# Performance work log

Hardware: AMD Instinct MI355X
Metric: run time of the kernel (lower is better)

The kernel has to match this reference:

```python
import jax, jax.numpy as jnp
import numpy as np

NJ, NS = 30000, 12000            # num job / skill nodes
E_JS, E_SJ, E_SS = 300000, 300000, 150000
SBERT, HID, OUT = 384, 128, 128
H = 2                             # GAT heads (concat=True)
NEG_SLOPE = 0.2


def setup_inputs() -> dict:
    key = jax.random.key(0)
    ks = iter(jax.random.split(key, 64))
    nrm = lambda shape, s=1.0: jax.random.normal(next(ks), shape, jnp.float32) * s
    ridx = lambda n, hi: jax.random.randint(next(ks), (n,), 0, hi, jnp.int32)
    W = 0.05  # weight scale to keep activations sane across layers
    return dict(
        x_job=nrm((NJ, SBERT)), x_skill=nrm((NS, SBERT)),
        ei_js_src=ridx(E_JS, NJ), ei_js_dst=ridx(E_JS, NS),
        ei_sj_src=ridx(E_SJ, NS), ei_sj_dst=ridx(E_SJ, NJ),
        ei_ss_src=ridx(E_SS, NS), ei_ss_dst=ridx(E_SS, NS),
        query=nrm((SBERT,)),
        W0_job=nrm((SBERT, HID), W), b0_job=jnp.zeros((HID,), jnp.float32),
        g0_job=jnp.ones((HID,), jnp.float32), be0_job=jnp.zeros((HID,), jnp.float32),
        W0_skill=nrm((SBERT, HID), W), b0_skill=jnp.zeros((HID,), jnp.float32),
        g0_skill=jnp.ones((HID,), jnp.float32), be0_skill=jnp.zeros((HID,), jnp.float32),
        gat_Ws=nrm((2, 3, HID, H * HID), W), gat_Wd=nrm((2, 3, HID, H * HID), W),
        gat_as=nrm((2, 3, H, HID), W), gat_ad=nrm((2, 3, H, HID), W),
        gat_b=jnp.zeros((2, 3, H * HID), jnp.float32),
        inter_W=nrm((2, 2, H * HID, HID), W), inter_b=jnp.zeros((2, 2, HID), jnp.float32),
        Wjf=nrm((HID, OUT), W), bjf=jnp.zeros((OUT,), jnp.float32),
        Wq=nrm((SBERT, OUT), W), bq=jnp.zeros((OUT,), jnp.float32),
    )


def _layer_norm(x, g, b):
    mu = x.mean(-1, keepdims=True)
    var = ((x - mu) ** 2).mean(-1, keepdims=True)
    return (x - mu) * jax.lax.rsqrt(var + 1e-5) * g + b


def _gat(x_src, x_dst, src, dst, Ws, Wd, a_s, a_d, bias, num_dst):
    # PyG GATConv: lin_src/lin_dst (no bias), additive attention, scatter-softmax over dst.
    hs = (x_src @ Ws).reshape(-1, H, HID)            # [Ns,H,C]
    hd = (x_dst @ Wd).reshape(-1, H, HID)            # [Nd,H,C]
    e = jax.nn.leaky_relu((hs * a_s).sum(-1)[src] + (hd * a_d).sum(-1)[dst], NEG_SLOPE)  # [E,H]
    m = jax.ops.segment_max(e, dst, num_segments=num_dst)
    p = jnp.exp(e - m[dst])
    den = jax.ops.segment_sum(p, dst, num_segments=num_dst)
    w = p / (den[dst] + 1e-16)                       # [E,H]
    out = jax.ops.segment_sum(hs[src] * w[:, :, None], dst, num_segments=num_dst)
    return out.reshape(num_dst, H * HID) + bias


def _forward(x_job, x_skill, query,
             W0_job, b0_job, g0_job, be0_job, W0_skill, b0_skill, g0_skill, be0_skill,
             gat_Ws, gat_Wd, gat_as, gat_ad, gat_b, inter_W, inter_b, Wjf, bjf, Wq, bq,
             ei_js_src, ei_js_dst, ei_sj_src, ei_sj_dst, ei_ss_src, ei_ss_dst):
    # initial per-type lin + LN + relu (dropout = identity in eval)
    xj = jax.nn.relu(_layer_norm(x_job @ W0_job + b0_job, g0_job, be0_job))
    xs = jax.nn.relu(_layer_norm(x_skill @ W0_skill + b0_skill, g0_skill, be0_skill))
    # skill->skill relation adds self loops (src == dst node type)
    loops = jnp.arange(NS, dtype=jnp.int32)
    ss_src = jnp.concatenate([ei_ss_src, loops])
    ss_dst = jnp.concatenate([ei_ss_dst, loops])
    for i in range(2):  # num_layers
        o_s = (_gat(xj, xs, ei_js_src, ei_js_dst, gat_Ws[i, 0], gat_Wd[i, 0],
                    gat_as[i, 0], gat_ad[i, 0], gat_b[i, 0], NS)
               + _gat(xs, xs, ss_src, ss_dst, gat_Ws[i, 2], gat_Wd[i, 2],
                      gat_as[i, 2], gat_ad[i, 2], gat_b[i, 2], NS))  # HeteroConv aggr='sum'
        o_j = _gat(xs, xj, ei_sj_src, ei_sj_dst, gat_Ws[i, 1], gat_Wd[i, 1],
                   gat_as[i, 1], gat_ad[i, 1], gat_b[i, 1], NJ)
        xj = jax.nn.relu(o_j @ inter_W[i, 0] + inter_b[i, 0])
        xs = jax.nn.relu(o_s @ inter_W[i, 1] + inter_b[i, 1])
    job_emb = xj @ Wjf + bjf                          # [NJ,OUT]
    q = query @ Wq + bq                               # [OUT]
    scores = job_emb @ q                              # [NJ]
    return scores, job_emb, q


def reference(x_job, x_skill, ei_js_src, ei_js_dst, ei_sj_src, ei_sj_dst,
              ei_ss_src, ei_ss_dst, query,
              W0_job, b0_job, g0_job, be0_job, W0_skill, b0_skill, g0_skill, be0_skill,
              gat_Ws, gat_Wd, gat_as, gat_ad, gat_b, inter_W, inter_b,
              Wjf, bjf, Wq, bq):
    return _forward(x_job, x_skill, query,
                    W0_job, b0_job, g0_job, be0_job, W0_skill, b0_skill, g0_skill, be0_skill,
                    gat_Ws, gat_Wd, gat_as, gat_ad, gat_b, inter_W, inter_b, Wjf, bjf, Wq, bq,
                    ei_js_src, ei_js_dst, ei_sj_src, ei_sj_dst, ei_ss_src, ei_ss_dst)
```

## Files before the change

kernel.cpp:

```cpp
#include <hip/hip_runtime.h>
#include <hip/hip_bf16.h>
#include <math.h>

#define NJ 30000
#define NS 12000
#define E_JS 300000
#define E_SJ 300000
#define E_SS 150000
#define ETOT (E_JS + E_SJ + E_SS + NS)
#define NBINS (NS + NJ + NS)
#define NBUK ((NBINS + 63) / 64)
#define SBERT 384
#define HIST_NB 512
#define SCAT_NB 120
#define CAST_MATS 10
#define CAST_BPM 48

static inline int cdiv(int a, int b) { return (a + b - 1) / b; }

typedef __attribute__((ext_vector_type(8))) short bf8_t;
typedef __attribute__((ext_vector_type(4))) float f4_t;
typedef unsigned short u16;

__device__ inline float bf2f(unsigned short u) {
    union { unsigned int i; float f; } z; z.i = ((unsigned int)u) << 16; return z.f;
}
__device__ inline unsigned short f2bf(float f) {
    unsigned int x = __float_as_uint(f);
    unsigned int r = (x + 0x7fffu + ((x >> 16) & 1u)) >> 16;
    return (unsigned short)r;
}

__device__ inline void edge_decode(int e, const int* js_src, const int* js_dst,
                                   const int* sj_src, const int* sj_dst,
                                   const int* ss_src, const int* ss_dst,
                                   int& src, int& bin) {
    if (e < E_JS) { src = js_src[e]; bin = js_dst[e]; }
    else if (e < E_JS + E_SJ) { int i = e - E_JS; src = sj_src[i]; bin = NS + sj_dst[i]; }
    else if (e < E_JS + E_SJ + E_SS) { int i = e - E_JS - E_SJ; src = ss_src[i]; bin = NS + NJ + ss_dst[i]; }
    else { int i = e - E_JS - E_SJ - E_SS; src = i; bin = NS + NJ + i; }
}

struct CastT { const float* src; unsigned short* dst; int K; int N; };
struct PrepArgs {
    CastT m[CAST_MATS];
    const float* Ws; const float* as_; const float* Wd; const float* ad_;
    float* wsa; float* wda; int* bcnt;
    const float* query; const float* Wq; const float* bq; float* qv;
};

__global__ __launch_bounds__(256) void k_prep(PrepArgs A) {
    __shared__ float ldt[32][33];
    int b = blockIdx.x;
    if (b < CAST_MATS * CAST_BPM) {
        int mi = b / CAST_BPM, bx = b % CAST_BPM;
        CastT cm = A.m[mi];
        int tilesN = cm.N >> 5;
        int total = (cm.K >> 5) * tilesN;
        if (bx >= total) return;
        int tk = bx / tilesN, tn = bx % tilesN;
        int k0 = tk * 32, n0 = tn * 32;
        int col = threadIdx.x & 31;
        int row0 = threadIdx.x >> 5;
#pragma unroll
        for (int r = 0; r < 4; ++r) {
            int kk = row0 + r * 8;
            ldt[kk][col] = cm.src[(size_t)(k0 + kk) * cm.N + n0 + col];
        }
        __syncthreads();
#pragma unroll
        for (int r = 0; r < 4; ++r) {
            int nn = row0 + r * 8;
            cm.dst[(size_t)(n0 + nn) * cm.K + k0 + col] = f2bf(ldt[col][nn]);
        }
    } else if (b < CAST_MATS * CAST_BPM + 12) {
        int id = (b - CAST_MATS * CAST_BPM) * 256 + threadIdx.x;
        if (id < NBUK) A.bcnt[id] = 0;
        if (id >= 2 * 1536) return;
        int which = id / 1536;
        int r = id % 1536;
        int lr = r / 256;
        int kh = r % 256;
        int k = kh / 2, h = kh % 2;
        const float* W = which ? A.Wd : A.Ws;
        const float* a = which ? A.ad_ : A.as_;
        const float* wrow = W + ((size_t)(lr * 128 + k)) * 256 + h * 128;
        const float* arow = a + (size_t)(lr * 2 + h) * 128;
        float acc = 0.f;
        for (int c2 = 0; c2 < 128; ++c2) acc += wrow[c2] * arow[c2];
        (which ? A.wda : A.wsa)[lr * 256 + k * 2 + h] = acc;
    } else {
        int c = threadIdx.x;
        if (c < 128) {
            float acc = A.bq[c];
            for (int k = 0; k < SBERT; ++k) acc += A.query[k] * A.Wq[(size_t)k * 128 + c];
            A.qv[c] = acc;
        }
    }
}

struct GJob {
    const void* X; const unsigned short* Wt;
    const float* bias; const float* gamma; const float* beta;
    void* Y; int M; int K; int N; int ldY; int srcf32;
    const float* qv; float* sc;
};
struct GPair { GJob a; GJob b; int blocksA; };

template <int EPI>
__device__ void mgemm_body(const GPair& P, int bx, int by) {
    int mb = bx;
    GJob g = (mb < P.blocksA) ? P.a : P.b;
    if (mb >= P.blocksA) mb -= P.blocksA;
    const int n0 = by * 128;
    if (n0 >= g.N) return;
    const int row0 = mb * 64;

    __shared__ __align__(16) unsigned short Al[64][40];
    __shared__ __align__(16) unsigned short Bl[128][40];
    const int t = threadIdx.x;
    const int wave = t >> 6, lane = t & 63;
    const int q = lane >> 4, c = lane & 15;
    const int K = g.K;

    f4_t acc[8];
#pragma unroll
    for (int nt = 0; nt < 8; ++nt) acc[nt] = (f4_t){0.f, 0.f, 0.f, 0.f};

    for (int k0 = 0; k0 < K; k0 += 32) {
#pragma unroll
        for (int it = 0; it < 3; ++it) {
            int idx = t + it * 256;
            int r = idx >> 2, cc = (idx & 3) * 8;
            if (r < 64) {
                int gr = row0 + r;
                if (g.srcf32) {
                    ushort4 lo = make_ushort4(0, 0, 0, 0), hi = lo;
                    if (gr < g.M) {
                        const float* Xf = (const float*)g.X;
                        const float* p = &Xf[(size_t)gr * K + k0 + cc];
                        float4 f0 = *(const float4*)p;
                        float4 f1 = *(const float4*)(p + 4);
                        lo = make_ushort4(f2bf(f0.x), f2bf(f0.y), f2bf(f0.z), f2bf(f0.w));
                        hi = make_ushort4(f2bf(f1.x), f2bf(f1.y), f2bf(f1.z), f2bf(f1.w));
                    }
                    *(ushort4*)&Al[r][cc] = lo;
                    *(ushort4*)&Al[r][cc + 4] = hi;
                } else {
                    const unsigned short* Xb = (const unsigned short*)g.X;
                    uint4 va = (gr < g.M) ? *(const uint4*)&Xb[(size_t)gr * K + k0 + cc]
                                          : make_uint4(0u, 0u, 0u, 0u);
                    *(uint4*)&Al[r][cc] = va;
                }
            } else {
                int br = r - 64;
                *(uint4*)&Bl[br][cc] = *(const uint4*)&g.Wt[(size_t)(n0 + br) * K + k0 + cc];
            }
        }
        __syncthreads();
        bf8_t af = *(const bf8_t*)&Al[wave * 16 + c][q * 8];
#pragma unroll
        for (int nt = 0; nt < 8; ++nt) {
            bf8_t bfr = *(const bf8_t*)&Bl[nt * 16 + c][q * 8];
            acc[nt] = __builtin_amdgcn_mfma_f32_16x16x32_bf16(af, bfr, acc[nt], 0, 0, 0);
        }
        __syncthreads();
    }

    float bcol[8], gcol[8], becol[8], qcol[8];
#pragma unroll
    for (int nt = 0; nt < 8; ++nt) {
        bcol[nt] = (EPI >= 1) ? g.bias[n0 + nt * 16 + c] : 0.f;
        if constexpr (EPI == 3) {
            gcol[nt] = g.gamma[nt * 16 + c];
            becol[nt] = g.beta[nt * 16 + c];
        }
        if constexpr (EPI == 1) qcol[nt] = g.qv[n0 + nt * 16 + c];
    }

#pragma unroll
    for (int r = 0; r < 4; ++r) {
        int grow = row0 + wave * 16 + q * 4 + r;
        float v[8];
#pragma unroll
        for (int nt = 0; nt < 8; ++nt) v[nt] = acc[nt][r] + bcol[nt];
        if constexpr (EPI == 3) {
            float s = 0.f, ss = 0.f;
#pragma unroll
            for (int nt = 0; nt < 8; ++nt) { s += v[nt]; ss += v[nt] * v[nt]; }
#pragma unroll
            for (int m = 8; m >= 1; m >>= 1) {
                s += __shfl_xor(s, m, 64);
                ss += __shfl_xor(ss, m, 64);
            }
            float mu = s * (1.f / 128.f);
            float var = ss * (1.f / 128.f) - mu * mu;
            float rs = rsqrtf(var + 1e-5f);
#pragma unroll
            for (int nt = 0; nt < 8; ++nt)
                v[nt] = fmaxf((v[nt] - mu) * rs * gcol[nt] + becol[nt], 0.f);
        } else if constexpr (EPI == 2) {
#pragma unroll
            for (int nt = 0; nt < 8; ++nt) v[nt] = fmaxf(v[nt], 0.f);
        }
        if constexpr (EPI == 1) {
            float part = 0.f;
#pragma unroll
            for (int nt = 0; nt < 8; ++nt) part += v[nt] * qcol[nt];
#pragma unroll
            for (int m = 8; m >= 1; m >>= 1) part += __shfl_xor(part, m, 64);
            if (c == 0 && grow < g.M) g.sc[grow] = part;
        }
        if (grow < g.M) {
            if constexpr (EPI == 1) {
                float* Y = (float*)g.Y;
#pragma unroll
                for (int nt = 0; nt < 8; ++nt)
                    Y[(size_t)grow * g.ldY + n0 + nt * 16 + c] = v[nt];
            } else {
                unsigned short* Y = (unsigned short*)g.Y;
#pragma unroll
                for (int nt = 0; nt < 8; ++nt)
                    Y[(size_t)grow * g.ldY + n0 + nt * 16 + c] = f2bf(v[nt]);
            }
        }
    }
}

template <int EPI>
__global__ __launch_bounds__(256) void k_mgemm(GPair P) {
    mgemm_body<EPI>(P, blockIdx.x, blockIdx.y);
}

__device__ void alpha_body(const unsigned short* xj, const unsigned short* xs,
                           const float* wsa, const float* wda, int l3,
                           float* aJ, float* aS, int b) {
    int wave = threadIdx.x >> 6, lane = threadIdx.x & 63;
    int node = b * 4 + wave;
    if (node < NJ) {
        ushort2 xv = *(const ushort2*)&xj[(size_t)node * 128 + lane * 2];
        float x0 = bf2f(xv.x), x1 = bf2f(xv.y);
        float4 w0 = *(const float4*)&wsa[(size_t)(l3 + 0) * 256 + lane * 4];
        float4 w1 = *(const float4*)&wda[(size_t)(l3 + 1) * 256 + lane * 4];
        float p0 = x0 * w0.x + x1 * w0.z, p1 = x0 * w0.y + x1 * w0.w;
        float p2 = x0 * w1.x + x1 * w1.z, p3 = x0 * w1.y + x1 * w1.w;
#pragma unroll
        for (int m = 32; m >= 1; m >>= 1) {
            p0 += __shfl_xor(p0, m, 64); p1 += __shfl_xor(p1, m, 64);
            p2 += __shfl_xor(p2, m, 64); p3 += __shfl_xor(p3, m, 64);
        }
        if (lane == 0) *(float4*)&aJ[(size_t)node * 4] = make_float4(p0, p1, p2, p3);
    } else if (node < NJ + NS) {
        int n = node - NJ;
        ushort2 xv = *(const ushort2*)&xs[(size_t)n * 128 + lane * 2];
        float x0 = bf2f(xv.x), x1 = bf2f(xv.y);
        float4 wA = *(const float4*)&wsa[(size_t)(l3 + 2) * 256 + lane * 4];
        float4 wB = *(const float4*)&wda[(size_t)(l3 + 0) * 256 + lane * 4];
        float4 wC = *(const float4*)&wsa[(size_t)(l3 + 1) * 256 + lane * 4];
        float4 wD = *(const float4*)&wda[(size_t)(l3 + 2) * 256 + lane * 4];
        float p0 = x0 * wA.x + x1 * wA.z, p1 = x0 * wA.y + x1 * wA.w;
        float p2 = x0 * wB.x + x1 * wB.z, p3 = x0 * wB.y + x1 * wB.w;
        float p4 = x0 * wC.x + x1 * wC.z, p5 = x0 * wC.y + x1 * wC.w;
        float p6 = x0 * wD.x + x1 * wD.z, p7 = x0 * wD.y + x1 * wD.w;
#pragma unroll
        for (int m = 32; m >= 1; m >>= 1) {
            p0 += __shfl_xor(p0, m, 64); p1 += __shfl_xor(p1, m, 64);
            p2 += __shfl_xor(p2, m, 64); p3 += __shfl_xor(p3, m, 64);
            p4 += __shfl_xor(p4, m, 64); p5 += __shfl_xor(p5, m, 64);
            p6 += __shfl_xor(p6, m, 64); p7 += __shfl_xor(p7, m, 64);
        }
        if (lane == 0) {
            float4* o = (float4*)&aS[(size_t)n * 8];
            o[0] = make_float4(p0, p1, p2, p3);
            o[1] = make_float4(p4, p5, p6, p7);
        }
    }
}

__global__ __launch_bounds__(256) void k_lin0_hist(
    GPair P, int gemmBlocks,
    const int* __restrict__ js_src, const int* __restrict__ js_dst,
    const int* __restrict__ sj_src, const int* __restrict__ sj_dst,
    const int* __restrict__ ss_src, const int* __restrict__ ss_dst,
    int* __restrict__ bcnt) {
    if (blockIdx.x < (unsigned)gemmBlocks) {
        mgemm_body<3>(P, blockIdx.x, blockIdx.y);
        return;
    }
    __shared__ int lh[NBUK];
    int t = threadIdx.x;
    for (int i = t; i < NBUK; i += 256) lh[i] = 0;
    __syncthreads();
    int hb = blockIdx.x - gemmBlocks;
    for (int e = hb * 256 + t; e < ETOT; e += HIST_NB * 256) {
        int src, bin;
        edge_decode(e, js_src, js_dst, sj_src, sj_dst, ss_src, ss_dst, src, bin);
        atomicAdd(&lh[bin >> 6], 1);
    }
    __syncthreads();
    for (int i = t; i < NBUK; i += 256) {
        int v = lh[i];
        if (v) atomicAdd(&bcnt[i], v);
    }
}

__global__ __launch_bounds__(256) void k_alpha_scan(
    const unsigned short* __restrict__ xj, const unsigned short* __restrict__ xs,
    const float* __restrict__ wsa, const float* __restrict__ wda, int l3,
    float* __restrict__ aJ, float* __restrict__ aS, int alphaBlocks,
    const int* __restrict__ bcnt, int* __restrict__ bukoff, int* __restrict__ bukcur) {
    if (blockIdx.x < (unsigned)alphaBlocks) {
        alpha_body(xj, xs, wsa, wda, l3, aJ, aS, blockIdx.x);
        return;
    }
    __shared__ int sd[256];
    int t = threadIdx.x;
    int i0 = t * 4;
    int v0 = (i0 < NBUK) ? bcnt[i0] : 0;
    int v1 = (i0 + 1 < NBUK) ? bcnt[i0 + 1] : 0;
    int v2 = (i0 + 2 < NBUK) ? bcnt[i0 + 2] : 0;
    int v3 = (i0 + 3 < NBUK) ? bcnt[i0 + 3] : 0;
    int csum = v0 + v1 + v2 + v3;
    sd[t] = csum;
    __syncthreads();
    for (int off = 1; off < 256; off <<= 1) {
        int tmp = (t >= off) ? sd[t - off] : 0;
        __syncthreads();
        sd[t] += tmp;
        __syncthreads();
    }
    int excl = sd[t] - csum;
    int p0 = excl, p1 = excl + v0, p2 = excl + v0 + v1, p3 = excl + v0 + v1 + v2;
    if (i0 < NBUK) { bukoff[i0] = p0; bukcur[i0] = p0; }
    if (i0 + 1 < NBUK) { bukoff[i0 + 1] = p1; bukcur[i0 + 1] = p1; }
    if (i0 + 2 < NBUK) { bukoff[i0 + 2] = p2; bukcur[i0 + 2] = p2; }
    if (i0 + 3 < NBUK) { bukoff[i0 + 3] = p3; bukcur[i0 + 3] = p3; }
    if (t == 0) bukoff[NBUK] = ETOT;
}

__global__ __launch_bounds__(256) void k_scatter_proj(
    GPair P, int gemmBlocks,
    const int* __restrict__ js_src, const int* __restrict__ js_dst,
    const int* __restrict__ sj_src, const int* __restrict__ sj_dst,
    const int* __restrict__ ss_src, const int* __restrict__ ss_dst,
    int* __restrict__ bukcur, uint2* __restrict__ pairs) {
    if (blockIdx.x < (unsigned)gemmBlocks) {
        mgemm_body<0>(P, blockIdx.x, blockIdx.y);
        return;
    }
    if (blockIdx.y != 0) return;
    __shared__ int lh[NBUK];
    __shared__ int lbase[NBUK];
    int t = threadIdx.x;
    int sb = blockIdx.x - gemmBlocks;
    const int CH = (ETOT + SCAT_NB - 1) / SCAT_NB;
    const int beg = sb * CH;
    const int endi = (beg + CH < ETOT) ? beg + CH : ETOT;
    for (int i = t; i < NBUK; i += 256) lh[i] = 0;
    __syncthreads();
    for (int e = beg + t; e < endi; e += 256) {
        int src, bin;
        edge_decode(e, js_src, js_dst, sj_src, sj_dst, ss_src, ss_dst, src, bin);
        atomicAdd(&lh[bin >> 6], 1);
    }
    __syncthreads();
    for (int i = t; i < NBUK; i += 256) {
        int v = lh[i];
        lbase[i] = v ? atomicAdd(&bukcur[i], v) : 0;
    }
    __syncthreads();
    for (int i = t; i < NBUK; i += 256) lh[i] = 0;
    __syncthreads();
    for (int e = beg + t; e < endi; e += 256) {
        int src, bin;
        edge_decode(e, js_src, js_dst, sj_src, sj_dst, ss_src, ss_dst, src, bin);
        int bu = bin >> 6;
        int pos = lbase[bu] + atomicAdd(&lh[bu], 1);
        pairs[pos] = make_uint2((unsigned)src, (unsigned)bin);
    }
}

__global__ __launch_bounds__(256) void k_proj_alpha(
    GPair P, int gemmBlocks,
    const unsigned short* __restrict__ xj, const unsigned short* __restrict__ xs,
    const float* __restrict__ wsa, const float* __restrict__ wda, int l3,
    float* __restrict__ aJ, float* __restrict__ aS) {
    if (blockIdx.x < (unsigned)gemmBlocks) {
        mgemm_body<0>(P, blockIdx.x, blockIdx.y);
        return;
    }
    if (blockIdx.y != 0) return;
    alpha_body(xj, xs, wsa, wda, l3, aJ, aS, blockIdx.x - gemmBlocks);
}

__global__ __launch_bounds__(256) void k_finalize(
    const uint2* __restrict__ pairs, const int* __restrict__ bukoff,
    int* __restrict__ offs, int* __restrict__ esrc) {
    int b = blockIdx.x, t = threadIdx.x;
    int base = bukoff[b], endi = bukoff[b + 1];
    __shared__ int cnt[64], excl[64], curs[64];
    if (t < 64) cnt[t] = 0;
    __syncthreads();
    for (int i = base + t; i < endi; i += 256)
        atomicAdd(&cnt[pairs[i].y & 63], 1);
    __syncthreads();
    if (t < 64) {
        int v = cnt[t];
        int inc = v;
#pragma unroll
        for (int off = 1; off < 64; off <<= 1) {
            int tmp = __shfl_up(inc, off, 64);
            if (t >= off) inc += tmp;
        }
        excl[t] = inc - v;
        curs[t] = inc - v;
    }
    __syncthreads();
    for (int i = base + t; i < endi; i += 256) {
        uint2 p = pairs[i];
        int lb = p.y & 63;
        int pos = atomicAdd(&curs[lb], 1);
        esrc[base + pos] = (int)p.x;
    }
    if (t < 64) {
        int bin = b * 64 + t;
        if (bin < NBINS) offs[bin] = base + excl[t];
    }
    if (b == 0 && t == 0) offs[NBINS] = ETOT;
}

__device__ inline void edge_accum(
    const int* __restrict__ esrc, int beg, int endi,
    const float* __restrict__ aSrc, int sStride, int hOff, float ad,
    const unsigned short* __restrict__ hs, int hsLd, int c,
    float& ax, float& ay, float& az, float& aw, float& den) {
    for (int j = beg; j < endi; j += 4) {
        int j1 = j + 1 < endi ? j + 1 : endi - 1;
        int j2 = j + 2 < endi ? j + 2 : endi - 1;
        int j3 = j + 3 < endi ? j + 3 : endi - 1;
        int s0 = esrc[j], s1 = esrc[j1], s2 = esrc[j2], s3 = esrc[j3];
        float as0 = aSrc[(size_t)s0 * sStride + hOff];
        float as1 = aSrc[(size_t)s1 * sStride + hOff];
        float as2 = aSrc[(size_t)s2 * sStride + hOff];
        float as3 = aSrc[(size_t)s3 * sStride + hOff];
        ushort4 v0 = *(const ushort4*)&hs[(size_t)s0 * hsLd + c];
        ushort4 v1 = *(const ushort4*)&hs[(size_t)s1 * hsLd + c];
        ushort4 v2 = *(const ushort4*)&hs[(size_t)s2 * hsLd + c];
        ushort4 v3 = *(const ushort4*)&hs[(size_t)s3 * hsLd + c];
        float e0 = as0 + ad; e0 = e0 > 0.f ? e0 : 0.2f * e0;
        float e1 = as1 + ad; e1 = e1 > 0.f ? e1 : 0.2f * e1;
        float e2 = as2 + ad; e2 = e2 > 0.f ? e2 : 0.2f * e2;
        float e3 = as3 + ad; e3 = e3 > 0.f ? e3 : 0.2f * e3;
        float p0 = __expf(e0);
        float p1 = (j + 1 < endi) ? __expf(e1) : 0.f;
        float p2 = (j + 2 < endi) ? __expf(e2) : 0.f;
        float p3 = (j + 3 < endi) ? __expf(e3) : 0.f;
        ax += p0 * bf2f(v0.x) + p1 * bf2f(v1.x) + p2 * bf2f(v2.x) + p3 * bf2f(v3.x);
        ay += p0 * bf2f(v0.y) + p1 * bf2f(v1.y) + p2 * bf2f(v2.y) + p3 * bf2f(v3.y);
        az += p0 * bf2f(v0.z) + p1 * bf2f(v1.z) + p2 * bf2f(v2.z) + p3 * bf2f(v3.z);
        aw += p0 * bf2f(v0.w) + p1 * bf2f(v1.w) + p2 * bf2f(v2.w) + p3 * bf2f(v3.w);
        den += p0 + p1 + p2 + p3;
    }
}

__global__ __launch_bounds__(256) void k_gather_all(
    const int* __restrict__ offs, const int* __restrict__ esrc,
    const float* __restrict__ aJ, const float* __restrict__ aS,
    const unsigned short* __restrict__ hs1, const unsigned short* __restrict__ hs2,
    const float* __restrict__ gb,
    unsigned short* __restrict__ oj, unsigned short* __restrict__ os,
    int jobOnly) {
    int wave = threadIdx.x >> 6, lane = threadIdx.x & 63;
    int idx = blockIdx.x * 4 + wave;
    int c = lane * 4;
    int h = (c >= 128) ? 1 : 0;
    if (jobOnly) {
        if (idx >= NJ) return;
        int d = idx;
        float ax = 0.f, ay = 0.f, az = 0.f, aw = 0.f, den = 0.f;
        int bb = NS + d;
        edge_accum(esrc, offs[bb], offs[bb + 1], aS, 8, 4 + h, aJ[(size_t)d * 4 + 2 + h],
                   hs2, 512, c, ax, ay, az, aw, den);
        float sc = 1.f / (den + 1e-16f);
        float4 b4 = *(const float4*)&gb[256 + c];
        float o0 = ax * sc + b4.x, o1 = ay * sc + b4.y;
        float o2 = az * sc + b4.z, o3 = aw * sc + b4.w;
        ushort4 o; o.x = f2bf(o0); o.y = f2bf(o1); o.z = f2bf(o2); o.w = f2bf(o3);
        *(ushort4*)&oj[(size_t)d * 256 + c] = o;
        return;
    }
    if (idx < NS) {
        int d = idx;
        float axA = 0.f, ayA = 0.f, azA = 0.f, awA = 0.f, denA = 0.f;
        edge_accum(esrc, offs[d], offs[d + 1], aJ, 4, h, aS[(size_t)d * 8 + 2 + h],
                   hs1, 256, c, axA, ayA, azA, awA, denA);
        float axB = 0.f, ayB = 0.f, azB = 0.f, awB = 0.f, denB = 0.f;
        int bb = NS + NJ + d;
        edge_accum(esrc, offs[bb], offs[bb + 1], aS, 8, h, aS[(size_t)d * 8 + 6 + h],
                   hs2 + 256, 512, c, axB, ayB, azB, awB, denB);
        float scA = 1.f / (denA + 1e-16f);
        float scB = 1.f / (denB + 1e-16f);
        float4 bA = *(const float4*)&gb[c];
        float4 bB = *(const float4*)&gb[512 + c];
        float o0 = axA * scA + bA.x + axB * scB + bB.x;
        float o1 = ayA * scA + bA.y + ayB * scB + bB.y;
        float o2 = azA * scA + bA.z + azB * scB + bB.z;
        float o3 = awA * scA + bA.w + awB * scB + bB.w;
        ushort4 o; o.x = f2bf(o0); o.y = f2bf(o1); o.z = f2bf(o2); o.w = f2bf(o3);
        *(ushort4*)&os[(size_t)d * 256 + c] = o;
    } else if (idx < NS + NJ) {
        int d = idx - NS;
        float ax = 0.f, ay = 0.f, az = 0.f, aw = 0.f, den = 0.f;
        int bb = NS + d;
        edge_accum(esrc, offs[bb], offs[bb + 1], aS, 8, 4 + h, aJ[(size_t)d * 4 + 2 + h],
                   hs2, 512, c, ax, ay, az, aw, den);
        float sc = 1.f / (den + 1e-16f);
        float4 b4 = *(const float4*)&gb[256 + c];
        float o0 = ax * sc + b4.x, o1 = ay * sc + b4.y;
        float o2 = az * sc + b4.z, o3 = aw * sc + b4.w;
        ushort4 o; o.x = f2bf(o0); o.y = f2bf(o1); o.z = f2bf(o2); o.w = f2bf(o3);
        *(ushort4*)&oj[(size_t)d * 256 + c] = o;
    }
}

extern "C" void kernel_launch(void* const* d_in, const int* in_sizes, int n_in,
                              void* d_out, int out_size, void* d_ws, size_t ws_size,
                              hipStream_t stream) {
    const float* x_job   = (const float*)d_in[0];
    const float* x_skill = (const float*)d_in[1];
    const int* js_src = (const int*)d_in[2];
    const int* js_dst = (const int*)d_in[3];
    const int* sj_src = (const int*)d_in[4];
    const int* sj_dst = (const int*)d_in[5];
    const int* ss_src = (const int*)d_in[6];
    const int* ss_dst = (const int*)d_in[7];
    const float* query    = (const float*)d_in[8];
    const float* W0_job   = (const float*)d_in[9];
    const float* b0_job   = (const float*)d_in[10];
    const float* g0_job   = (const float*)d_in[11];
    const float* be0_job  = (const float*)d_in[12];
    const float* W0_skill = (const float*)d_in[13];
    const float* b0_skill = (const float*)d_in[14];
    const float* g0_skill = (const float*)d_in[15];
    const float* be0_skill= (const float*)d_in[16];
    const float* gat_Ws = (const float*)d_in[17];
    const float* gat_Wd = (const float*)d_in[18];
    const float* gat_as = (const float*)d_in[19];
    const float* gat_ad = (const float*)d_in[20];
    const float* gat_b  = (const float*)d_in[21];
    const float* inter_W = (const float*)d_in[22];
    const float* inter_b = (const float*)d_in[23];
    const float* Wjf = (const float*)d_in[24];
    const float* bjf = (const float*)d_in[25];
    const float* Wq  = (const float*)d_in[26];
    const float* bq  = (const float*)d_in[27];

    char* w = (char*)d_ws;
    auto alloc = [&](size_t bytes) -> void* {
        void* p = (void*)w;
        w += (bytes + 255) & ~(size_t)255;
        return p;
    };
    u16* xj  = (u16*)alloc((size_t)NJ * 128 * 2);
    u16* xs  = (u16*)alloc((size_t)NS * 128 * 2);
    u16* hs1 = (u16*)alloc((size_t)NJ * 256 * 2);
    u16* hs2 = (u16*)alloc((size_t)NS * 512 * 2);
    u16* oj  = (u16*)alloc((size_t)NJ * 256 * 2);
    u16* os  = (u16*)alloc((size_t)NS * 256 * 2);
    u16* WtW0j = (u16*)alloc((size_t)SBERT * 128 * 2);
    u16* WtW0s = (u16*)alloc((size_t)SBERT * 128 * 2);
    u16* WtWs  = (u16*)alloc((size_t)6 * 128 * 256 * 2);
    u16* WtI   = (u16*)alloc((size_t)4 * 256 * 128 * 2);
    u16* WtJf  = (u16*)alloc((size_t)128 * 128 * 2);
    float* aJ = (float*)alloc((size_t)NJ * 4 * 4);
    float* aS = (float*)alloc((size_t)NS * 8 * 4);
    float* wsa = (float*)alloc(6 * 256 * 4);
    float* wda = (float*)alloc(6 * 256 * 4);
    int* bcnt   = (int*)alloc((size_t)NBUK * 4);
    int* bukoff = (int*)alloc((size_t)(NBUK + 1) * 4);
    int* bukcur = (int*)alloc((size_t)NBUK * 4);
    uint2* pairs = (uint2*)alloc((size_t)ETOT * 8);
    int* offs = (int*)alloc((size_t)(NBINS + 1) * 4);
    int* esrc = (int*)alloc((size_t)ETOT * 4);

    float* out = (float*)d_out;
    float* scores  = out;
    float* job_emb = out + NJ;
    float* qv      = out + NJ + (size_t)NJ * 128;

    const int mbJ = cdiv(NJ, 64);
    const int mbS = cdiv(NS, 64);
    const int gemmB = mbJ + mbS;
    const int alphaB = cdiv(NJ + NS, 4);

    {
        PrepArgs A;
        A.m[0] = {W0_job, WtW0j, SBERT, 128};
        A.m[1] = {W0_skill, WtW0s, SBERT, 128};
        A.m[2] = {gat_Ws + (size_t)0 * 128 * 256, WtWs + (size_t)0 * 256 * 128, 128, 256};
        A.m[3] = {gat_Ws + (size_t)1 * 128 * 256, WtWs + (size_t)1 * 256 * 128, 128, 256};
        A.m[4] = {gat_Ws + (size_t)2 * 128 * 256, WtWs + (size_t)2 * 256 * 128, 128, 256};
        A.m[5] = {gat_Ws + (size_t)4 * 128 * 256, WtWs + (size_t)4 * 256 * 128, 128, 256};
        A.m[6] = {inter_W + (size_t)0 * 256 * 128, WtI + (size_t)0 * 128 * 256, 256, 128};
        A.m[7] = {inter_W + (size_t)1 * 256 * 128, WtI + (size_t)1 * 128 * 256, 256, 128};
        A.m[8] = {inter_W + (size_t)2 * 256 * 128, WtI + (size_t)2 * 128 * 256, 256, 128};
        A.m[9] = {Wjf, WtJf, 128, 128};
        A.Ws = gat_Ws; A.as_ = gat_as; A.Wd = gat_Wd; A.ad_ = gat_ad;
        A.wsa = wsa; A.wda = wda; A.bcnt = bcnt;
        A.query = query; A.Wq = Wq; A.bq = bq; A.qv = qv;
        k_prep<<<CAST_MATS * CAST_BPM + 12 + 1, 256, 0, stream>>>(A);
    }

    {
        GPair P;
        P.a = {x_job, WtW0j, b0_job, g0_job, be0_job, xj, NJ, SBERT, 128, 128, 1, nullptr, nullptr};
        P.b = {x_skill, WtW0s, b0_skill, g0_skill, be0_skill, xs, NS, SBERT, 128, 128, 1, nullptr, nullptr};
        P.blocksA = mbJ;
        k_lin0_hist<<<dim3(gemmB + HIST_NB, 1), 256, 0, stream>>>(
            P, gemmB, js_src, js_dst, sj_src, sj_dst, ss_src, ss_dst, bcnt);
    }

    k_alpha_scan<<<alphaB + 1, 256, 0, stream>>>(xj, xs, wsa, wda, 0, aJ, aS,
                                                 alphaB, bcnt, bukoff, bukcur);

    {
        GPair P;
        P.a = {xj, WtWs + (size_t)0 * 256 * 128, nullptr, nullptr, nullptr,
               hs1, NJ, 128, 256, 256, 0, nullptr, nullptr};
        P.b = {xs, WtWs + (size_t)1 * 256 * 128, nullptr, nullptr, nullptr,
               hs2, NS, 128, 512, 512, 0, nullptr, nullptr};
        P.blocksA = mbJ;
        k_scatter_proj<<<dim3(gemmB + SCAT_NB, 4), 256, 0, stream>>>(
            P, gemmB, js_src, js_dst, sj_src, sj_dst, ss_src, ss_dst, bukcur, pairs);
    }

    k_finalize<<<NBUK, 256, 0, stream>>>(pairs, bukoff, offs, esrc);

    k_gather_all<<<cdiv(NS + NJ, 4), 256, 0, stream>>>(
        offs, esrc, aJ, aS, hs1, hs2, gat_b + 0, oj, os, 0);

    {
        GPair P;
        P.a = {oj, WtI + (size_t)0 * 128 * 256, inter_b + 0,
               nullptr, nullptr, xj, NJ, 256, 128, 128, 0, nullptr, nullptr};
        P.b = {os, WtI + (size_t)1 * 128 * 256, inter_b + 128,
               nullptr, nullptr, xs, NS, 256, 128, 128, 0, nullptr, nullptr};
        P.blocksA = mbJ;
        k_mgemm<2><<<dim3(gemmB, 1), 256, 0, stream>>>(P);
    }

    {
        GPair P;
        P.a = {xs, WtWs + (size_t)4 * 256 * 128, nullptr, nullptr, nullptr,
               hs2, NS, 128, 256, 512, 0, nullptr, nullptr};
        P.b = P.a;
        P.blocksA = mbS;
        k_proj_alpha<<<dim3(mbS + alphaB, 2), 256, 0, stream>>>(
            P, mbS, xj, xs, wsa, wda, 3, aJ, aS);
    }

    k_gather_all<<<cdiv(NJ, 4), 256, 0, stream>>>(
        offs, esrc, aJ, aS, hs1, hs2, gat_b + (size_t)3 * 256, oj, os, 1);

    {
        GPair P;
        P.a = {oj, WtI + (size_t)2 * 128 * 256, inter_b + 2 * 128,
               nullptr, nullptr, xj, NJ, 256, 128, 128, 0, nullptr, nullptr};
        P.b = P.a;
        P.blocksA = mbJ;
        k_mgemm<2><<<dim3(mbJ, 1), 256, 0, stream>>>(P);
    }

    {
        GPair P;
        P.a = {xj, WtJf, bjf, nullptr, nullptr, job_emb, NJ, 128, 128, 128, 0, qv, scores};
        P.b = P.a;
        P.blocksA = mbJ;
        k_mgemm<1><<<dim3(mbJ, 1), 256, 0, stream>>>(P);
    }
}
```

Measured before the change: 365.4 us.

## Fuse attention-logit projections into GEMM epilogues and chain back-to-back GEMMs

Attention logits (alpha) are now computed in the epilogues of the lin0 and inter GEMMs, which removes the separate alpha kernels and their re-reads of xj/xs. The edge histogram moves into the prep kernel, and a memset zeroes the bucket counters. A new k_fused2 kernel chains the inter linear with the next projection (layer-2 Ws for skills, final Wjf plus the score dot for jobs) through shared memory, so the intermediate activations are never written to or read back from global memory. This cuts about three launches, at the cost of extra LDS use and register pressure in the fused GEMM.

```diff
diff --git a/kernel.cpp b/kernel.cpp
--- a/kernel.cpp
+++ b/kernel.cpp
@@ -15,6 +15,10 @@
 #define SCAT_NB 120
 #define CAST_MATS 10
 #define CAST_BPM 48
+#define PREP_CAST (CAST_MATS * CAST_BPM)
+#define PREP_WA   (PREP_CAST + 12)
+#define PREP_QV   PREP_WA
+#define PREP_HIST (PREP_QV + 1)
 
 static inline int cdiv(int a, int b) { return (a + b - 1) / b; }
 
@@ -47,12 +51,16 @@
     const float* Ws; const float* as_; const float* Wd; const float* ad_;
     float* wsa; float* wda; int* bcnt;
     const float* query; const float* Wq; const float* bq; float* qv;
+    const int* js_src; const int* js_dst;
+    const int* sj_src; const int* sj_dst;
+    const int* ss_src; const int* ss_dst;
 };
 
 __global__ __launch_bounds__(256) void k_prep(PrepArgs A) {
     __shared__ float ldt[32][33];
+    __shared__ int lh[NBUK];
     int b = blockIdx.x;
-    if (b < CAST_MATS * CAST_BPM) {
+    if (b < PREP_CAST) {
         int mi = b / CAST_BPM, bx = b % CAST_BPM;
         CastT cm = A.m[mi];
         int tilesN = cm.N >> 5;
@@ -73,9 +81,8 @@
             int nn = row0 + r * 8;
             cm.dst[(size_t)(n0 + nn) * cm.K + k0 + col] = f2bf(ldt[col][nn]);
         }
-    } else if (b < CAST_MATS * CAST_BPM + 12) {
-        int id = (b - CAST_MATS * CAST_BPM) * 256 + threadIdx.x;
-        if (id < NBUK) A.bcnt[id] = 0;
+    } else if (b < PREP_WA) {
+        int id = (b - PREP_CAST) * 256 + threadIdx.x;
         if (id >= 2 * 1536) return;
         int which = id / 1536;
         int r = id % 1536;
@@ -89,13 +96,28 @@
         float acc = 0.f;
         for (int c2 = 0; c2 < 128; ++c2) acc += wrow[c2] * arow[c2];
         (which ? A.wda : A.wsa)[lr * 256 + k * 2 + h] = acc;
-    } else {
+    } else if (b == PREP_QV) {
         int c = threadIdx.x;
         if (c < 128) {
             float acc = A.bq[c];
             for (int k = 0; k < SBERT; ++k) acc += A.query[k] * A.Wq[(size_t)k * 128 + c];
             A.qv[c] = acc;
         }
+    } else {
+        int t = threadIdx.x;
+        for (int i = t; i < NBUK; i += 256) lh[i] = 0;
+        __syncthreads();
+        int hb = b - PREP_HIST;
+        for (int e = hb * 256 + t; e < ETOT; e += HIST_NB * 256) {
+            int src, bin;
+            edge_decode(e, A.js_src, A.js_dst, A.sj_src, A.sj_dst, A.ss_src, A.ss_dst, src, bin);
+            atomicAdd(&lh[bin >> 6], 1);
+        }
+        __syncthreads();
+        for (int i = t; i < NBUK; i += 256) {
+            int v = lh[i];
+            if (v) atomicAdd(&A.bcnt[i], v);
+        }
     }
 }
 
@@ -104,6 +126,10 @@
     const float* bias; const float* gamma; const float* beta;
     void* Y; int M; int K; int N; int ldY; int srcf32;
     const float* qv; float* sc;
+    int aMode = 0;
+    const float* wav0 = nullptr; const float* wav1 = nullptr;
+    const float* wav2 = nullptr; const float* wav3 = nullptr;
+    float* aOut = nullptr; int aStride = 0;
 };
 struct GPair { GJob a; GJob b; int blocksA; };
 
@@ -211,6 +237,40 @@
             for (int m = 8; m >= 1; m >>= 1) part += __shfl_xor(part, m, 64);
             if (c == 0 && grow < g.M) g.sc[grow] = part;
         }
+        if (g.aMode > 0) {
+            float pa[8];
+#pragma unroll
+            for (int i = 0; i < 8; ++i) pa[i] = 0.f;
+#pragma unroll
+            for (int nt = 0; nt < 8; ++nt) {
+                int col = nt * 16 + c;
+                float2 w0 = *(const float2*)&g.wav0[col * 2];
+                pa[0] += v[nt] * w0.x; pa[1] += v[nt] * w0.y;
+                if (g.aMode > 1) {
+                    float2 w1 = *(const float2*)&g.wav1[col * 2];
+                    pa[2] += v[nt] * w1.x; pa[3] += v[nt] * w1.y;
+                }
+                if (g.aMode > 2) {
+                    float2 w2 = *(const float2*)&g.wav2[col * 2];
+                    float2 w3 = *(const float2*)&g.wav3[col * 2];
+                    pa[4] += v[nt] * w2.x; pa[5] += v[nt] * w2.y;
+                    pa[6] += v[nt] * w3.x; pa[7] += v[nt] * w3.y;
+                }
+            }
+#pragma unroll
+            for (int m = 8; m >= 1; m >>= 1) {
+                pa[0] += __shfl_xor(pa[0], m, 64); pa[1] += __shfl_xor(pa[1], m, 64);
+                pa[2] += __shfl_xor(pa[2], m, 64); pa[3] += __shfl_xor(pa[3], m, 64);
+                pa[4] += __shfl_xor(pa[4], m, 64); pa[5] += __shfl_xor(pa[5], m, 64);
+                pa[6] += __shfl_xor(pa[6], m, 64); pa[7] += __shfl_xor(pa[7], m, 64);
+            }
+            if (c == 0 && grow < g.M) {
+                float* ao = &g.aOut[(size_t)grow * g.aStride];
+                ao[0] = pa[0]; ao[1] = pa[1];
+                if (g.aMode > 1) { ao[2] = pa[2]; ao[3] = pa[3]; }
+                if (g.aMode > 2) { ao[4] = pa[4]; ao[5] = pa[5]; ao[6] = pa[6]; ao[7] = pa[7]; }
+            }
+        }
         if (grow < g.M) {
             if constexpr (EPI == 1) {
                 float* Y = (float*)g.Y;
@@ -232,85 +292,11 @@
     mgemm_body<EPI>(P, blockIdx.x, blockIdx.y);
 }
 
-__device__ void alpha_body(const unsigned short* xj, const unsigned short* xs,
-                           const float* wsa, const float* wda, int l3,
-                           float* aJ, float* aS, int b) {
-    int wave = threadIdx.x >> 6, lane = threadIdx.x & 63;
-    int node = b * 4 + wave;
-    if (node < NJ) {
-        ushort2 xv = *(const ushort2*)&xj[(size_t)node * 128 + lane * 2];
-        float x0 = bf2f(xv.x), x1 = bf2f(xv.y);
-        float4 w0 = *(const float4*)&wsa[(size_t)(l3 + 0) * 256 + lane * 4];
-        float4 w1 = *(const float4*)&wda[(size_t)(l3 + 1) * 256 + lane * 4];
-        float p0 = x0 * w0.x + x1 * w0.z, p1 = x0 * w0.y + x1 * w0.w;
-        float p2 = x0 * w1.x + x1 * w1.z, p3 = x0 * w1.y + x1 * w1.w;
-#pragma unroll
-        for (int m = 32; m >= 1; m >>= 1) {
-            p0 += __shfl_xor(p0, m, 64); p1 += __shfl_xor(p1, m, 64);
-            p2 += __shfl_xor(p2, m, 64); p3 += __shfl_xor(p3, m, 64);
-        }
-        if (lane == 0) *(float4*)&aJ[(size_t)node * 4] = make_float4(p0, p1, p2, p3);
-    } else if (node < NJ + NS) {
-        int n = node - NJ;
-        ushort2 xv = *(const ushort2*)&xs[(size_t)n * 128 + lane * 2];
-        float x0 = bf2f(xv.x), x1 = bf2f(xv.y);
-        float4 wA = *(const float4*)&wsa[(size_t)(l3 + 2) * 256 + lane * 4];
-        float4 wB = *(const float4*)&wda[(size_t)(l3 + 0) * 256 + lane * 4];
-        float4 wC = *(const float4*)&wsa[(size_t)(l3 + 1) * 256 + lane * 4];
-        float4 wD = *(const float4*)&wda[(size_t)(l3 + 2) * 256 + lane * 4];
-        float p0 = x0 * wA.x + x1 * wA.z, p1 = x0 * wA.y + x1 * wA.w;
-        float p2 = x0 * wB.x + x1 * wB.z, p3 = x0 * wB.y + x1 * wB.w;
-        float p4 = x0 * wC.x + x1 * wC.z, p5 = x0 * wC.y + x1 * wC.w;
-        float p6 = x0 * wD.x + x1 * wD.z, p7 = x0 * wD.y + x1 * wD.w;
-#pragma unroll
-        for (int m = 32; m >= 1; m >>= 1) {
-            p0 += __shfl_xor(p0, m, 64); p1 += __shfl_xor(p1, m, 64);
-            p2 += __shfl_xor(p2, m, 64); p3 += __shfl_xor(p3, m, 64);
-            p4 += __shfl_xor(p4, m, 64); p5 += __shfl_xor(p5, m, 64);
-            p6 += __shfl_xor(p6, m, 64); p7 += __shfl_xor(p7, m, 64);
-        }
-        if (lane == 0) {
-            float4* o = (float4*)&aS[(size_t)n * 8];
-            o[0] = make_float4(p0, p1, p2, p3);
-            o[1] = make_float4(p4, p5, p6, p7);
-        }
-    }
-}
-
-__global__ __launch_bounds__(256) void k_lin0_hist(
+__global__ __launch_bounds__(256) void k_lin0_scan(
     GPair P, int gemmBlocks,
-    const int* __restrict__ js_src, const int* __restrict__ js_dst,
-    const int* __restrict__ sj_src, const int* __restrict__ sj_dst,
-    const int* __restrict__ ss_src, const int* __restrict__ ss_dst,
-    int* __restrict__ bcnt) {
+    const int* __restrict__ bcnt, int* __restrict__ bukoff, int* __restrict__ bukcur) {
     if (blockIdx.x < (unsigned)gemmBlocks) {
-        mgemm_body<3>(P, blockIdx.x, blockIdx.y);
-        return;
-    }
-    __shared__ int lh[NBUK];
-    int t = threadIdx.x;
-    for (int i = t; i < NBUK; i += 256) lh[i] = 0;
-    __syncthreads();
-    int hb = blockIdx.x - gemmBlocks;
-    for (int e = hb * 256 + t; e < ETOT; e += HIST_NB * 256) {
-        int src, bin;
-        edge_decode(e, js_src, js_dst, sj_src, sj_dst, ss_src, ss_dst, src, bin);
-        atomicAdd(&lh[bin >> 6], 1);
-    }
-    __syncthreads();
-    for (int i = t; i < NBUK; i += 256) {
-        int v = lh[i];
-        if (v) atomicAdd(&bcnt[i], v);
-    }
-}
-
-__global__ __launch_bounds__(256) void k_alpha_scan(
-    const unsigned short* __restrict__ xj, const unsigned short* __restrict__ xs,
-    const float* __restrict__ wsa, const float* __restrict__ wda, int l3,
-    float* __restrict__ aJ, float* __restrict__ aS, int alphaBlocks,
-    const int* __restrict__ bcnt, int* __restrict__ bukoff, int* __restrict__ bukcur) {
-    if (blockIdx.x < (unsigned)alphaBlocks) {
-        alpha_body(xj, xs, wsa, wda, l3, aJ, aS, blockIdx.x);
+        mgemm_body<3>(P, blockIdx.x, 0);
         return;
     }
     __shared__ int sd[256];
@@ -378,19 +364,6 @@
         int pos = lbase[bu] + atomicAdd(&lh[bu], 1);
         pairs[pos] = make_uint2((unsigned)src, (unsigned)bin);
     }
-}
-
-__global__ __launch_bounds__(256) void k_proj_alpha(
-    GPair P, int gemmBlocks,
-    const unsigned short* __restrict__ xj, const unsigned short* __restrict__ xs,
-    const float* __restrict__ wsa, const float* __restrict__ wda, int l3,
-    float* __restrict__ aJ, float* __restrict__ aS) {
-    if (blockIdx.x < (unsigned)gemmBlocks) {
-        mgemm_body<0>(P, blockIdx.x, blockIdx.y);
-        return;
-    }
-    if (blockIdx.y != 0) return;
-    alpha_body(xj, xs, wsa, wda, l3, aJ, aS, blockIdx.x - gemmBlocks);
 }
 
 __global__ __launch_bounds__(256) void k_finalize(
@@ -466,7 +439,9 @@
 __global__ __launch_bounds__(256) void k_gather_all(
     const int* __restrict__ offs, const int* __restrict__ esrc,
     const float* __restrict__ aJ, const float* __restrict__ aS,
-    const unsigned short* __restrict__ hs1, const unsigned short* __restrict__ hs2,
+    const unsigned short* __restrict__ hs1,
+    const unsigned short* __restrict__ hsss, int ssLd,
+    const unsigned short* __restrict__ hsj, int sjLd,
     const float* __restrict__ gb,
     unsigned short* __restrict__ oj, unsigned short* __restrict__ os,
     int jobOnly) {
@@ -480,7 +455,7 @@
         float ax = 0.f, ay = 0.f, az = 0.f, aw = 0.f, den = 0.f;
         int bb = NS + d;
         edge_accum(esrc, offs[bb], offs[bb + 1], aS, 8, 4 + h, aJ[(size_t)d * 4 + 2 + h],
-                   hs2, 512, c, ax, ay, az, aw, den);
+                   hsj, sjLd, c, ax, ay, az, aw, den);
         float sc = 1.f / (den + 1e-16f);
         float4 b4 = *(const float4*)&gb[256 + c];
         float o0 = ax * sc + b4.x, o1 = ay * sc + b4.y;
@@ -497,7 +472,7 @@
         float axB = 0.f, ayB = 0.f, azB = 0.f, awB = 0.f, denB = 0.f;
         int bb = NS + NJ + d;
         edge_accum(esrc, offs[bb], offs[bb + 1], aS, 8, h, aS[(size_t)d * 8 + 6 + h],
-                   hs2 + 256, 512, c, axB, ayB, azB, awB, denB);
+                   hsss, ssLd, c, axB, ayB, azB, awB, denB);
         float scA = 1.f / (denA + 1e-16f);
         float scB = 1.f / (denB + 1e-16f);
         float4 bA = *(const float4*)&gb[c];
@@ -513,13 +488,154 @@
         float ax = 0.f, ay = 0.f, az = 0.f, aw = 0.f, den = 0.f;
         int bb = NS + d;
         edge_accum(esrc, offs[bb], offs[bb + 1], aS, 8, 4 + h, aJ[(size_t)d * 4 + 2 + h],
-                   hs2, 512, c, ax, ay, az, aw, den);
+                   hsj, sjLd, c, ax, ay, az, aw, den);
         float sc = 1.f / (den + 1e-16f);
         float4 b4 = *(const float4*)&gb[256 + c];
         float o0 = ax * sc + b4.x, o1 = ay * sc + b4.y;
         float o2 = az * sc + b4.z, o3 = aw * sc + b4.w;
         ushort4 o; o.x = f2bf(o0); o.y = f2bf(o1); o.z = f2bf(o2); o.w = f2bf(o3);
         *(ushort4*)&oj[(size_t)d * 256 + c] = o;
+    }
+}
+
+struct FJob {
+    const unsigned short* X; const unsigned short* Wt1; const float* bias1;
+    int M; int K1;
+    const float* wa; float* aOut; int aStride;
+    const unsigned short* Wt2; const float* bias2; int N2;
+    void* Y2; int ldY2; int y2f32;
+    const float* qv; float* sc;
+};
+struct FPair { FJob a; FJob b; int blocksA; };
+
+__global__ __launch_bounds__(256) void k_fused2(FPair P) {
+    int mb = blockIdx.x;
+    FJob g = (mb < P.blocksA) ? P.a : P.b;
+    if (mb >= P.blocksA) mb -= P.blocksA;
+    const int row0 = mb * 64;
+
+    __shared__ __align__(16) unsigned short Al[64][40];
+    __shared__ __align__(16) unsigned short Bl[128][40];
+    __shared__ __align__(16) unsigned short Y1l[4][64][40];
+    const int t = threadIdx.x;
+    const int wave = t >> 6, lane = t & 63;
+    const int q = lane >> 4, c = lane & 15;
+
+    f4_t acc[8];
+#pragma unroll
+    for (int nt = 0; nt < 8; ++nt) acc[nt] = (f4_t){0.f, 0.f, 0.f, 0.f};
+
+    for (int k0 = 0; k0 < g.K1; k0 += 32) {
+#pragma unroll
+        for (int it = 0; it < 3; ++it) {
+            int idx = t + it * 256;
+            int r = idx >> 2, cc = (idx & 3) * 8;
+            if (r < 64) {
+                int gr = row0 + r;
+                uint4 va = (gr < g.M) ? *(const uint4*)&g.X[(size_t)gr * g.K1 + k0 + cc]
+                                      : make_uint4(0u, 0u, 0u, 0u);
+                *(uint4*)&Al[r][cc] = va;
+            } else {
+                int br = r - 64;
+                *(uint4*)&Bl[br][cc] = *(const uint4*)&g.Wt1[(size_t)br * g.K1 + k0 + cc];
+            }
+        }
+        __syncthreads();
+        bf8_t af = *(const bf8_t*)&Al[wave * 16 + c][q * 8];
+#pragma unroll
+        for (int nt = 0; nt < 8; ++nt) {
+            bf8_t bfr = *(const bf8_t*)&Bl[nt * 16 + c][q * 8];
+            acc[nt] = __builtin_amdgcn_mfma_f32_16x16x32_bf16(af, bfr, acc[nt], 0, 0, 0);
+        }
+        __syncthreads();
+    }
+
+    float bcol[8];
+#pragma unroll
+    for (int nt = 0; nt < 8; ++nt) bcol[nt] = g.bias1[nt * 16 + c];
+#pragma unroll
+    for (int r = 0; r < 4; ++r) {
+        int row = wave * 16 + q * 4 + r;
+        int grow = row0 + row;
+        float v[8];
+#pragma unroll
+        for (int nt = 0; nt < 8; ++nt) v[nt] = fmaxf(acc[nt][r] + bcol[nt], 0.f);
+        if (g.wa) {
+            float pa0 = 0.f, pa1 = 0.f;
+#pragma unroll
+            for (int nt = 0; nt < 8; ++nt) {
+                float2 w0 = *(const float2*)&g.wa[(nt * 16 + c) * 2];
+                pa0 += v[nt] * w0.x; pa1 += v[nt] * w0.y;
+            }
+#pragma unroll
+            for (int m = 8; m >= 1; m >>= 1) {
+                pa0 += __shfl_xor(pa0, m, 64);
+                pa1 += __shfl_xor(pa1, m, 64);
+            }
+            if (c == 0 && grow < g.M) {
+                g.aOut[(size_t)grow * g.aStride + 0] = pa0;
+                g.aOut[(size_t)grow * g.aStride + 1] = pa1;
+            }
+        }
+#pragma unroll
+        for (int nt = 0; nt < 8; ++nt)
+            Y1l[nt >> 1][row][(nt & 1) * 16 + c] = f2bf(v[nt]);
+    }
+    if (g.N2 == 0) return;
+    __syncthreads();
+
+    for (int n2 = 0; n2 < g.N2; n2 += 128) {
+        f4_t acc2[8];
+#pragma unroll
+        for (int nt = 0; nt < 8; ++nt) acc2[nt] = (f4_t){0.f, 0.f, 0.f, 0.f};
+        for (int k0 = 0; k0 < 128; k0 += 32) {
+#pragma unroll
+            for (int it = 0; it < 2; ++it) {
+                int idx = t + it * 256;
+                int br = idx >> 2, cc = (idx & 3) * 8;
+                *(uint4*)&Bl[br][cc] = *(const uint4*)&g.Wt2[(size_t)(n2 + br) * 128 + k0 + cc];
+            }
+            __syncthreads();
+            bf8_t af = *(const bf8_t*)&Y1l[k0 >> 5][wave * 16 + c][q * 8];
+#pragma unroll
+            for (int nt = 0; nt < 8; ++nt) {
+                bf8_t bfr = *(const bf8_t*)&Bl[nt * 16 + c][q * 8];
+                acc2[nt] = __builtin_amdgcn_mfma_f32_16x16x32_bf16(af, bfr, acc2[nt], 0, 0, 0);
+            }
+            __syncthreads();
+        }
+        float b2[8], qcol[8];
+#pragma unroll
+        for (int nt = 0; nt < 8; ++nt) {
+            b2[nt] = g.bias2 ? g.bias2[n2 + nt * 16 + c] : 0.f;
+            if (g.y2f32) qcol[nt] = g.qv[n2 + nt * 16 + c];
+        }
+#pragma unroll
+        for (int r = 0; r < 4; ++r) {
+            int grow = row0 + wave * 16 + q * 4 + r;
+            float v[8];
+#pragma unroll
+            for (int nt = 0; nt < 8; ++nt) v[nt] = acc2[nt][r] + b2[nt];
+            if (g.y2f32) {
+                float part = 0.f;
+#pragma unroll
+                for (int nt = 0; nt < 8; ++nt) part += v[nt] * qcol[nt];
+#pragma unroll
+                for (int m = 8; m >= 1; m >>= 1) part += __shfl_xor(part, m, 64);
+                if (c == 0 && grow < g.M) g.sc[grow] = part;
+                if (grow < g.M) {
+                    float* Y = (float*)g.Y2;
+#pragma unroll
+                    for (int nt = 0; nt < 8; ++nt)
+                        Y[(size_t)grow * g.ldY2 + n2 + nt * 16 + c] = v[nt];
+                }
+            } else if (grow < g.M) {
+                unsigned short* Y = (unsigned short*)g.Y2;
+#pragma unroll
+                for (int nt = 0; nt < 8; ++nt)
+                    Y[(size_t)grow * g.ldY2 + n2 + nt * 16 + c] = f2bf(v[nt]);
+            }
+        }
     }
 }
 
@@ -565,6 +681,7 @@
     u16* xs  = (u16*)alloc((size_t)NS * 128 * 2);
     u16* hs1 = (u16*)alloc((size_t)NJ * 256 * 2);
     u16* hs2 = (u16*)alloc((size_t)NS * 512 * 2);
+    u16* hs3 = (u16*)alloc((size_t)NS * 256 * 2);
     u16* oj  = (u16*)alloc((size_t)NJ * 256 * 2);
     u16* os  = (u16*)alloc((size_t)NS * 256 * 2);
     u16* WtW0j = (u16*)alloc((size_t)SBERT * 128 * 2);
@@ -591,7 +708,8 @@
     const int mbJ = cdiv(NJ, 64);
     const int mbS = cdiv(NS, 64);
     const int gemmB = mbJ + mbS;
-    const int alphaB = cdiv(NJ + NS, 4);
+
+    hipMemsetAsync(bcnt, 0, (size_t)NBUK * 4, stream);
 
     {
         PrepArgs A;
@@ -608,20 +726,21 @@
         A.Ws = gat_Ws; A.as_ = gat_as; A.Wd = gat_Wd; A.ad_ = gat_ad;
         A.wsa = wsa; A.wda = wda; A.bcnt = bcnt;
         A.query = query; A.Wq = Wq; A.bq = bq; A.qv = qv;
-        k_prep<<<CAST_MATS * CAST_BPM + 12 + 1, 256, 0, stream>>>(A);
+        A.js_src = js_src; A.js_dst = js_dst;
+        A.sj_src = sj_src; A.sj_dst = sj_dst;
+        A.ss_src = ss_src; A.ss_dst = ss_dst;
+        k_prep<<<PREP_HIST + HIST_NB, 256, 0, stream>>>(A);
     }
 
     {
         GPair P;
-        P.a = {x_job, WtW0j, b0_job, g0_job, be0_job, xj, NJ, SBERT, 128, 128, 1, nullptr, nullptr};
-        P.b = {x_skill, WtW0s, b0_skill, g0_skill, be0_skill, xs, NS, SBERT, 128, 128, 1, nullptr, nullptr};
+        P.a = {x_job, WtW0j, b0_job, g0_job, be0_job, xj, NJ, SBERT, 128, 128, 1,
+               nullptr, nullptr, 2, wsa + 0, wda + 256, nullptr, nullptr, aJ, 4};
+        P.b = {x_skill, WtW0s, b0_skill, g0_skill, be0_skill, xs, NS, SBERT, 128, 128, 1,
+               nullptr, nullptr, 4, wsa + 2 * 256, wda + 0, wsa + 1 * 256, wda + 2 * 256, aS, 8};
         P.blocksA = mbJ;
-        k_lin0_hist<<<dim3(gemmB + HIST_NB, 1), 256, 0, stream>>>(
-            P, gemmB, js_src, js_dst, sj_src, sj_dst, ss_src, ss_dst, bcnt);
-    }
-
-    k_alpha_scan<<<alphaB + 1, 256, 0, stream>>>(xj, xs, wsa, wda, 0, aJ, aS,
-                                                 alphaB, bcnt, bukoff, bukcur);
+        k_lin0_scan<<<dim3(gemmB + 1, 1), 256, 0, stream>>>(P, gemmB, bcnt, bukoff, bukcur);
+    }
 
     {
         GPair P;
@@ -637,45 +756,31 @@
     k_finalize<<<NBUK, 256, 0, stream>>>(pairs, bukoff, offs, esrc);
 
     k_gather_all<<<cdiv(NS + NJ, 4), 256, 0, stream>>>(
-        offs, esrc, aJ, aS, hs1, hs2, gat_b + 0, oj, os, 0);
+        offs, esrc, aJ, aS, hs1, hs2 + 256, 512, hs2, 512, gat_b, oj, os, 0);
 
     {
-        GPair P;
-        P.a = {oj, WtI + (size_t)0 * 128 * 256, inter_b + 0,
-               nullptr, nullptr, xj, NJ, 256, 128, 128, 0, nullptr, nullptr};
-        P.b = {os, WtI + (size_t)1 * 128 * 256, inter_b + 128,
-               nullptr, nullptr, xs, NS, 256, 128, 128, 0, nullptr, nullptr};
+        FPair P;
+        P.a = {oj, WtI + (size_t)0 * 128 * 256, inter_b + 0, NJ, 256,
+               wda + (size_t)4 * 256, aJ + 2, 4,
+               nullptr, nullptr, 0, nullptr, 0, 0, nullptr, nullptr};
+        P.b = {os, WtI + (size_t)1 * 128 * 256, inter_b + 128, NS, 256,
+               wsa + (size_t)4 * 256, aS + 4, 8,
+               WtWs + (size_t)4 * 256 * 128, nullptr, 256, hs3, 256, 0, nullptr, nullptr};
         P.blocksA = mbJ;
-        k_mgemm<2><<<dim3(gemmB, 1), 256, 0, stream>>>(P);
-    }
+        k_fused2<<<dim3(gemmB, 1), 256, 0, stream>>>(P);
+    }
+
+    k_gather_all<<<cdiv(NJ, 4), 256, 0, stream>>>(
+        offs, esrc, aJ, aS, nullptr, nullptr, 0, hs3, 256,
+        gat_b + (size_t)3 * 256, oj, nullptr, 1);
 
     {
-        GPair P;
-        P.a = {xs, WtWs + (size_t)4 * 256 * 128, nullptr, nullptr, nullptr,
-               hs2, NS, 128, 256, 512, 0, nullptr, nullptr};
-        P.b = P.a;
-        P.blocksA = mbS;
-        k_proj_alpha<<<dim3(mbS + alphaB, 2), 256, 0, stream>>>(
-            P, mbS, xj, xs, wsa, wda, 3, aJ, aS);
-    }
-
-    k_gather_all<<<cdiv(NJ, 4), 256, 0, stream>>>(
-        offs, esrc, aJ, aS, hs1, hs2, gat_b + (size_t)3 * 256, oj, os, 1);
-
-    {
-        GPair P;
-        P.a = {oj, WtI + (size_t)2 * 128 * 256, inter_b + 2 * 128,
-               nullptr, nullptr, xj, NJ, 256, 128, 128, 0, nullptr, nullptr};
+        FPair P;
+        P.a = {oj, WtI + (size_t)2 * 128 * 256, inter_b + 2 * 128, NJ, 256,
+               nullptr, nullptr, 0,
+               WtJf, bjf, 128, job_emb, 128, 1, qv, scores};
         P.b = P.a;
         P.blocksA = mbJ;
-        k_mgemm<2><<<dim3(mbJ, 1), 256, 0, stream>>>(P);
-    }
-
-    {
-        GPair P;
-        P.a = {xj, WtJf, bjf, nullptr, nullptr, job_emb, NJ, 128, 128, 128, 0, qv, scores};
-        P.b = P.a;
-        P.blocksA = mbJ;
-        k_mgemm<1><<<dim3(mbJ, 1), 256, 0, stream>>>(P);
-    }
-}
+        k_fused2<<<dim3(mbJ, 1), 256, 0, stream>>>(P);
+    }
+}
```

New measurement: 344.3 us. 5.8% less time.
